# Kernel tuning notes

Hardware: AMD Instinct MI355X
Metric: run time of the kernel (lower is better)

Reference implementation:

```python
import jax, jax.numpy as jnp
import numpy as np

B, DIM, RANK, H, W = 16, 64, 32, 128, 128
E, K, BINS, FREQ_DIM, KS = 4, 2, 8, 64, 7
NOISE_STD = 1.0 / E


def dwconv(x, w, b, pad):
    # depthwise conv, NCHW, weight [C,1,kh,kw]
    y = jax.lax.conv_general_dilated(x, w, (1, 1), [(pad, pad), (pad, pad)],
        dimension_numbers=('NCHW', 'OIHW', 'NCHW'), feature_group_count=x.shape[1])
    return y + b[None, :, None, None]


def avgpool3(x):
    # AvgPool2d(3, stride=1, padding=1), count_include_pad=True -> sum/9
    s = jax.lax.reduce_window(x, 0.0, jax.lax.add, (1, 1, 3, 3), (1, 1, 1, 1),
        [(0, 0), (0, 0), (1, 1), (1, 1)])
    return s / 9.0


def freq_filter(x, gain, decay, cmax):
    # HighFreqGlobal / LowFreqGlobal: rfft2 -> scale magnitude by radial filter -> irfft2
    Bh, C, Hh, Wh = x.shape
    xf = jnp.fft.rfft2(x, norm='ortho')
    mag, ph = jnp.abs(xf), jnp.angle(xf)
    fy = jnp.fft.fftfreq(Hh).astype(x.dtype)[:, None]
    fx = jnp.fft.rfftfreq(Wh).astype(x.dtype)[None, :]
    fg = jnp.sqrt(fy ** 2 + fx ** 2)
    filt = jnp.clip((1.0 - jnp.exp(-gain * fg)) * jnp.exp(-decay * fg), 0.0, cmax)
    return jnp.fft.irfft2((mag * filt) * jnp.exp(1j * ph), s=(Hh, Wh), norm='ortho')


def freq_energy(x):
    # RoutingFunction.get_frequency_energy: radial energy histogram over BINS bins
    Bh, C, Hh, Wh = x.shape
    mag = jnp.abs(jnp.fft.fft2(x, norm='forward'))
    gy = jnp.arange(-Hh // 2, Hh // 2, dtype=jnp.float32)[:, None]
    gx = jnp.arange(-Wh // 2, Wh // 2, dtype=jnp.float32)[None, :]
    dist = jnp.sqrt(gy ** 2 + gx ** 2)
    edges = jnp.linspace(0.0, dist.max(), BINS + 1)
    masks = ((dist[None] >= edges[:-1, None, None]) & (dist[None] < edges[1:, None, None])).astype(mag.dtype)
    return jnp.einsum('bchw,khw->bk', mag, masks) / C  # sum over HW then mean over C


def setup_inputs():
    key = jax.random.key(0)
    ks = jax.random.split(key, 16)
    p = lambda k, shp, s=0.02: jax.random.normal(k, shp, jnp.float32) * s
    return {
        'x': jax.random.normal(ks[0], (B, DIM, H, W), jnp.float32),
        'noise': jax.random.normal(ks[1], (B, E), jnp.float32),
        'gate_w': p(ks[2], (E, DIM)),
        'fg_w1': p(ks[3], (FREQ_DIM, BINS)),
        'fg_b1': jnp.zeros((FREQ_DIM,), jnp.float32),
        'fg_w2': p(ks[4], (E, FREQ_DIM)),
        'proj0': p(ks[5], (E, RANK, DIM)),
        'proj1': p(ks[6], (E, RANK, DIM)),
        'proj2': p(ks[7], (E, DIM, RANK)),
        'hg_gain': jnp.float32(2.0),
        'hg_decay': jnp.float32(0.5),
        'hf_w1': p(ks[8], (RANK, 1, 3, 3), 0.1),
        'hf_b1': jnp.zeros((RANK,), jnp.float32),
        'hf_w2': p(ks[9], (RANK, 1, 3, 3), 0.1),
        'hf_b2': jnp.zeros((RANK,), jnp.float32),
        'lg_gain': jnp.float32(1.0),
        'lg_decay': jnp.float32(1.0),
        'lf_w': p(ks[10], (RANK, 1, KS, KS), 0.1),
        'lf_b': jnp.zeros((RANK,), jnp.float32),
    }


def reference(x, noise, gate_w, fg_w1, fg_b1, fg_w2, proj0, proj1, proj2,
              hg_gain, hg_decay, hf_w1, hf_b1, hf_w2, hf_b2,
              lg_gain, lg_decay, lf_w, lf_b):
    Bh = x.shape[0]
    # routing: image gate (GAP + linear) + frequency gate (MLP on radial energy)
    img_logits = jnp.mean(x, axis=(2, 3)) @ gate_w.T
    femb = freq_energy(x)
    hidden = jax.nn.relu(femb @ fg_w1.T + fg_b1)
    logits = img_logits + hidden @ fg_w2.T
    scores = jax.nn.softmax(logits + noise * NOISE_STD, axis=-1)
    vals, idx = jax.lax.top_k(scores, K)
    gates = jnp.zeros_like(scores).at[jnp.arange(Bh)[:, None], idx].set(vals)

    def expert(e, body):
        # ModExpert.process: low-rank proj -> body * silu(gate proj of shared=x) -> up proj + shortcut
        h = jnp.einsum('bchw,rc->brhw', x, proj0[e])
        g = jax.nn.silu(jnp.einsum('bchw,rc->brhw', x, proj1[e]))
        h = body(h) * g
        return jnp.einsum('brhw,cr->bchw', h, proj2[e]) + x

    gelu = lambda z: jax.nn.gelu(z, approximate=False)
    bodies = [
        lambda z: freq_filter(z, hg_gain, hg_decay, 3.0),                          # HighFreqGlobal
        lambda z: dwconv(gelu(dwconv(z, hf_w1, hf_b1, 1)), hf_w2, hf_b2, 1),       # HighFreqLocal
        lambda z: freq_filter(z, lg_gain, lg_decay, 1.0),                          # LowFreqGlobal
        lambda z: avgpool3(gelu(dwconv(z, lf_w, lf_b, KS // 2))),                  # LowFreqLocal
    ]
    # dispatch/combine expressed densely: gates are exactly zero for non-selected experts,
    # so weighted sum == SparseDispatcher.combine
    out = jnp.zeros_like(x)
    for e, body in enumerate(bodies):
        out = out + gates[:, e][:, None, None, None] * expert(e, body)
    return out
```

## Files before the change

kernel.cpp:

```cpp
#include <hip/hip_runtime.h>
#include <math.h>


namespace {

struct cpx { float x, y; };
struct TwB {
  cpx t0;
  cpx ws[6];
  float sg[6];
};

using bf16x8 = __attribute__((ext_vector_type(8))) short;
using f32x4  = __attribute__((ext_vector_type(4))) float;

__device__ __forceinline__ short f2bf(float f){
  unsigned u = __float_as_uint(f);
  u += 0x7FFF + ((u >> 16) & 1);
  return (short)(u >> 16);
}

__device__ __forceinline__ cpx cmul(cpx a, cpx b){ return {a.x*b.x - a.y*b.y, a.x*b.y + a.y*b.x}; }

__device__ __forceinline__ void init_twb(TwB &T, int lane, const float2* __restrict__ tw128){
  float2 v0 = tw128[lane];
  T.t0 = {v0.x, v0.y};
  int m = 32;
  #pragma unroll
  for (int s = 0; s < 6; s++){
    bool up = (lane & m) != 0;
    float2 wv = tw128[(lane & (m-1)) * (64/m)];
    T.ws[s] = up ? cpx{wv.x, wv.y} : cpx{1.0f, 0.0f};
    T.sg[s] = up ? -1.0f : 1.0f;
    m >>= 1;
  }
}

__device__ __forceinline__ int br6(int l){ return (int)(__brev((unsigned)l) >> 26); }
__device__ __forceinline__ int pos7(int j){ return ((j & 1) << 6) | (j >> 1); }

__device__ __forceinline__ void fft128(cpx &a, cpx &b, int lane, const TwB &T){
  cpx u{a.x + b.x, a.y + b.y};
  cpx v{a.x - b.x, a.y - b.y};
  v = cmul(v, T.t0);
  a = u; b = v;
  int m = 32;
  #pragma unroll
  for (int s = 0; s < 6; s++){
    float pax = __shfl_xor(a.x, m);
    float pay = __shfl_xor(a.y, m);
    float pbx = __shfl_xor(b.x, m);
    float pby = __shfl_xor(b.y, m);
    float sg = T.sg[s];
    cpx w = T.ws[s];
    cpx ta{fmaf(sg, a.x, pax), fmaf(sg, a.y, pay)};
    cpx tb{fmaf(sg, b.x, pbx), fmaf(sg, b.y, pby)};
    a = cmul(ta, w);
    b = cmul(tb, w);
    m >>= 1;
  }
}

__device__ __forceinline__ float gelu_exact(float v){
  return 0.5f * v * (1.0f + erff(v * 0.70710678118654752f));
}

__device__ __forceinline__ float silu(float v){
  return v / (1.0f + expf(-v));
}


__global__ __launch_bounds__(512) void k_fft2fwd(const float* __restrict__ x, float2* __restrict__ X,
                                                 float* __restrict__ part_w, float* __restrict__ xmean){
  __shared__ float2 z[8192];
  int bc = blockIdx.x; int t = threadIdx.x;
  int lane = t & 63, wv = t >> 6;
  if (t < 128){
    float s, c;
    sincosf(-6.283185307179586f * (float)t * (1.0f/128.0f), &s, &c);
    z[t] = make_float2(c, s);
  }
  __syncthreads();
  TwB T; init_twb(T, lane, (const float2*)z);
  __syncthreads();
  const float* img = x + (size_t)bc * 16384;
  int rb = br6(lane);

  #pragma unroll 4
  for (int k = 0; k < 8; k++){
    int p = wv*8 + k;
    int h0 = 2*p, h1 = 2*p + 1;
    cpx a{img[h0*128 + lane],      img[h1*128 + lane]};
    cpx b{img[h0*128 + lane + 64], img[h1*128 + lane + 64]};
    fft128(a, b, lane, T);
    int ia = (p << 7) | (rb ^ p);
    z[ia]      = make_float2(a.x, a.y);
    z[ia | 64] = make_float2(b.x, b.y);
  }
  __syncthreads();

  float rax[8], ray[8], rbx[8], rby[8];
  #pragma unroll
  for (int k = 0; k < 8; k++){
    int jj = wv*8 + k;
    int p  = lane >> 1, s = lane & 1;
    int p2 = 32 + p;
    cpx a, b;
    if (jj == 0){
      float2 z0  = z[(p << 7)  | (0  ^ p)];
      float2 z64 = z[(p << 7)  | (32 ^ p)];
      float2 w0  = z[(p2 << 7) | (0  ^ p2)];
      float2 w64 = z[(p2 << 7) | (32 ^ p2)];
      a = { s ? z0.y : z0.x, s ? z64.y : z64.x };
      b = { s ? w0.y : w0.x, s ? w64.y : w64.x };
    } else {
      int jm = 128 - jj;
      int pj = pos7(jj), pm = pos7(jm);
      float2 z1 = z[(p << 7) | (pj ^ p)],  z2 = z[(p << 7) | (pm ^ p)];
      if (s == 0) a = { 0.5f*(z1.x + z2.x), 0.5f*(z1.y - z2.y) };
      else        a = { 0.5f*(z1.y + z2.y), 0.5f*(z2.x - z1.x) };
      float2 w1 = z[(p2 << 7) | (pj ^ p2)], w2 = z[(p2 << 7) | (pm ^ p2)];
      if (s == 0) b = { 0.5f*(w1.x + w2.x), 0.5f*(w1.y - w2.y) };
      else        b = { 0.5f*(w1.y + w2.y), 0.5f*(w2.x - w1.x) };
    }
    fft128(a, b, lane, T);
    rax[k] = a.x; ray[k] = a.y; rbx[k] = b.x; rby[k] = b.y;
  }
  __syncthreads();
  #pragma unroll
  for (int k = 0; k < 8; k++){
    int jj = wv*8 + k;
    int ia = (jj << 7) | (rb ^ jj);
    z[ia]      = make_float2(rax[k], ray[k]);
    z[ia | 64] = make_float2(rbx[k], rby[k]);
  }
  __syncthreads();

  if (t == 0) xmean[bc] = z[0].x * (1.0f/16384.0f);

  float edges[9];
  float step = sqrtf(8192.0f) * 0.125f;
  #pragma unroll
  for (int k = 0; k <= 8; k++) edges[k] = step * (float)k;
  float acc[8] = {0,0,0,0,0,0,0,0};
  for (int idx = t; idx < 64*128; idx += 512){
    int j = idx >> 7, i = idx & 127;
    if (j == 0){
      float2 c0 = z[pos7(i)];
      int in_ = (128 - i) & 127;
      float2 d0v = z[pos7(in_)];
      float x0r = 0.5f*(c0.x + d0v.x), x0i = 0.5f*(c0.y - d0v.y);
      float x6r = 0.5f*(c0.y + d0v.y), x6i = 0.5f*(d0v.x - c0.x);
      float m0 = sqrtf(x0r*x0r + x0i*x0i) * (1.0f/16384.0f);
      float m6 = sqrtf(x6r*x6r + x6i*x6i) * (1.0f/16384.0f);
      float dyv = (float)(i - 64);
      float d0 = sqrtf(dyv*dyv + 4096.0f);
      float d6 = fabsf(dyv);
      #pragma unroll
      for (int k = 0; k < 8; k++){
        if (d0 >= edges[k] && d0 < edges[k+1]) acc[k] += m0;
        if (d6 >= edges[k] && d6 < edges[k+1]) acc[k] += m6;
      }
    } else {
      float2 zv = z[(j << 7) | (pos7(i) ^ j)];
      float mag = sqrtf(zv.x*zv.x + zv.y*zv.y) * (2.0f/16384.0f);
      float dy = (float)(i - 64), dx = (float)(j - 64);
      float d = sqrtf(dy*dy + dx*dx);
      #pragma unroll
      for (int k = 0; k < 8; k++)
        if (d >= edges[k] && d < edges[k+1]) acc[k] += mag;
    }
  }
  #pragma unroll
  for (int k = 0; k < 8; k++){
    float v = acc[k];
    for (int off = 32; off > 0; off >>= 1) v += __shfl_xor(v, off);
    if (lane == 0) part_w[(bc*8 + wv)*8 + k] = v;
  }

  float2* Xo = X + (size_t)bc * (65*128);
  for (int idx = t; idx < 65*128; idx += 512){
    int j = idx >> 7, i = idx & 127;
    float2 v;
    if (j == 0){
      float2 c0 = z[pos7(i)];
      int in_ = (128 - i) & 127;
      float2 d0v = z[pos7(in_)];
      v = make_float2(0.5f*(c0.x + d0v.x), 0.5f*(c0.y - d0v.y));
    } else if (j == 64){
      float2 c0 = z[pos7(i)];
      int in_ = (128 - i) & 127;
      float2 d0v = z[pos7(in_)];
      v = make_float2(0.5f*(c0.y + d0v.y), 0.5f*(d0v.x - c0.x));
    } else {
      v = z[(j << 7) | (pos7(i) ^ j)];
    }
    Xo[idx] = v;
  }
}

__global__ __launch_bounds__(128) void k_routing(const float* __restrict__ xmean, const float* __restrict__ part_w,
    const float* __restrict__ noise, const float* __restrict__ gate_w,
    const float* __restrict__ fg_w1, const float* __restrict__ fg_b1, const float* __restrict__ fg_w2,
    const float* __restrict__ proj0, float* __restrict__ p0t,
    int* __restrict__ slot_e, int* __restrict__ slot_of, float* __restrict__ slot_g){
  __shared__ float femb[16][8];
  __shared__ float hid[16][64];
  __shared__ float lgt[16][4];
  int t = threadIdx.x;
  for (int idx = t; idx < 2048; idx += 128){
    int r = idx >> 6, c = idx & 63;
    p0t[0*2048 + c*32 + r] = proj0[0*2048 + idx];
    p0t[1*2048 + c*32 + r] = proj0[2*2048 + idx];
  }
  {
    int b = t >> 3, k = t & 7;
    float s = 0.f;
    for (int c = 0; c < 64; c++)
      for (int w = 0; w < 8; w++)
        s += part_w[((b*64 + c)*8 + w)*8 + k];
    femb[b][k] = s * (1.0f/64.0f);
  }
  __syncthreads();
  for (int idx = t; idx < 16*64; idx += 128){
    int b = idx >> 6, f = idx & 63;
    float s = fg_b1[f];
    for (int k = 0; k < 8; k++) s += femb[b][k] * fg_w1[f*8 + k];
    hid[b][f] = fmaxf(s, 0.f);
  }
  __syncthreads();
  if (t < 64){
    int b = t >> 2, e = t & 3;
    float s = 0.f;
    for (int c = 0; c < 64; c++) s += xmean[b*64 + c] * gate_w[e*64 + c];
    for (int f = 0; f < 64; f++) s += hid[b][f] * fg_w2[e*64 + f];
    lgt[b][e] = s + noise[b*4 + e] * 0.25f;
  }
  __syncthreads();
  if (t < 16){
    int b = t;
    float m = fmaxf(fmaxf(lgt[b][0], lgt[b][1]), fmaxf(lgt[b][2], lgt[b][3]));
    float p[4]; float sum = 0.f;
    for (int e = 0; e < 4; e++){ p[e] = expf(lgt[b][e] - m); sum += p[e]; }
    for (int e = 0; e < 4; e++) p[e] /= sum;
    int i1 = 0;
    for (int e = 1; e < 4; e++) if (p[e] > p[i1]) i1 = e;
    int i2 = -1;
    for (int e = 0; e < 4; e++){ if (e == i1) continue; if (i2 < 0 || p[e] > p[i2]) i2 = e; }
    slot_e[b*2 + 0] = i1;
    slot_e[b*2 + 1] = i2;
    slot_g[b*2 + 0] = p[i1];
    slot_g[b*2 + 1] = p[i2];
    for (int e = 0; e < 4; e++) slot_of[b*4 + e] = (e == i1) ? 0 : ((e == i2) ? 1 : -1);
  }
}

__global__ __launch_bounds__(256) void k_projfreq(const float2* __restrict__ X, const float* __restrict__ p0t,
    float2* __restrict__ Y, const int* __restrict__ slot_e,
    const float* __restrict__ hg_gain, const float* __restrict__ hg_decay,
    const float* __restrict__ lg_gain, const float* __restrict__ lg_decay){
  int b = blockIdx.z;
  int e0 = __builtin_amdgcn_readfirstlane(slot_e[b*2 + 0]);
  int e1 = __builtin_amdgcn_readfirstlane(slot_e[b*2 + 1]);
  bool f0 = (e0 == 0) || (e0 == 2);
  bool f1 = (e1 == 0) || (e1 == 2);
  if (!f0 && !f1) return;
  int j = blockIdx.y;
  int i0 = blockIdx.x * 64;
  int t = threadIdx.x;
  int lane = t & 63;
  int w = __builtin_amdgcn_readfirstlane(t >> 6);
  __shared__ float2 sx[64][64];
  for (int idx = t; idx < 4096; idx += 256){
    int c = idx >> 6, ii = idx & 63;
    sx[c][ii] = X[(((size_t)(b*64 + c))*65 + j)*128 + i0 + ii];
  }
  __syncthreads();
  int i = i0 + lane;
  const float* W0 = p0t + ((f0 ? (e0 >> 1) : (e1 >> 1)) * 2048) + w*8;
  const float* W1 = p0t + ((f1 ? (e1 >> 1) : (e0 >> 1)) * 2048) + w*8;
  float a0x[8] = {0,0,0,0,0,0,0,0}, a0y[8] = {0,0,0,0,0,0,0,0};
  float a1x[8] = {0,0,0,0,0,0,0,0}, a1y[8] = {0,0,0,0,0,0,0,0};
  for (int c = 0; c < 64; c++){
    float2 xv = sx[c][lane];
    const float* wc0 = W0 + c*32;
    const float* wc1 = W1 + c*32;
    #pragma unroll
    for (int k = 0; k < 8; k++){
      float w0v = wc0[k];
      a0x[k] += w0v * xv.x; a0y[k] += w0v * xv.y;
      float w1v = wc1[k];
      a1x[k] += w1v * xv.x; a1y[k] += w1v * xv.y;
    }
  }
  float fy = (float)(i < 64 ? i : i - 128) * (1.0f/128.0f);
  float fx = (float)j * (1.0f/128.0f);
  float fg = sqrtf(fy*fy + fx*fx);
  if (f0){
    float gain, decay, cmax;
    if (e0 == 0){ gain = *hg_gain; decay = *hg_decay; cmax = 3.0f; }
    else        { gain = *lg_gain; decay = *lg_decay; cmax = 1.0f; }
    float filt = (1.0f - expf(-gain*fg)) * expf(-decay*fg);
    filt = fminf(fmaxf(filt, 0.0f), cmax) * (1.0f/16384.0f);
    int bs = b*2 + 0;
    #pragma unroll
    for (int k = 0; k < 8; k++){
      int r = w*8 + k;
      Y[((size_t)(bs*32 + r))*8320 + j*128 + i] = make_float2(a0x[k]*filt, a0y[k]*filt);
    }
  }
  if (f1){
    float gain, decay, cmax;
    if (e1 == 0){ gain = *hg_gain; decay = *hg_decay; cmax = 3.0f; }
    else        { gain = *lg_gain; decay = *lg_decay; cmax = 1.0f; }
    float filt = (1.0f - expf(-gain*fg)) * expf(-decay*fg);
    filt = fminf(fmaxf(filt, 0.0f), cmax) * (1.0f/16384.0f);
    int bs = b*2 + 1;
    #pragma unroll
    for (int k = 0; k < 8; k++){
      int r = w*8 + k;
      Y[((size_t)(bs*32 + r))*8320 + j*128 + i] = make_float2(a1x[k]*filt, a1y[k]*filt);
    }
  }
}

__global__ __launch_bounds__(512) void k_ifta(float2* __restrict__ Y, const int* __restrict__ slot_e,
    const float* __restrict__ x, const float* __restrict__ proj0, float* __restrict__ A){
  __shared__ __align__(16) unsigned char ubuf[65536];
  int bid = blockIdx.x;
  int t = threadIdx.x;
  if (bid < 1024){
    int bs = bid >> 5, r = bid & 31;
    int es = slot_e[bs];
    if (es == 1 || es == 3) return;
    float2* z = (float2*)ubuf;
    int lane = t & 63, wv = t >> 6;
    if (t < 128){
      float s, c;
      sincosf(-6.283185307179586f * (float)t * (1.0f/128.0f), &s, &c);
      z[t] = make_float2(c, s);
    }
    __syncthreads();
    TwB T; init_twb(T, lane, (const float2*)z);
    __syncthreads();
    int rb = br6(lane);
    float2* Yb = Y + (size_t)(bs*32 + r) * 8320;

    for (int idx = t; idx < 8192; idx += 512){
      int j = idx >> 7, i = idx & 127;
      if (j == 0){
        float2 y0 = Yb[i];
        float2 y6 = Yb[8192 + i];
        z[pos7(i)] = make_float2(y0.x - y6.y, y0.y + y6.x);
      } else {
        z[(j << 7) | (pos7(i) ^ j)] = Yb[idx];
      }
    }
    __syncthreads();

    #pragma unroll
    for (int k = 0; k < 8; k++){
      int jj = wv*8 + k;
      float2 z0 = z[(jj << 7) | (pos7(lane) ^ jj)];
      float2 z1 = z[(jj << 7) | ((pos7(lane) + 32) ^ jj)];
      cpx a{z0.x, -z0.y}, b{z1.x, -z1.y};
      fft128(a, b, lane, T);
      int ia = (jj << 7) | (rb ^ jj);
      z[ia]      = make_float2(a.x, -a.y);
      z[ia | 64] = make_float2(b.x, -b.y);
    }
    __syncthreads();

    float* body = (float*)Yb;
    #pragma unroll 2
    for (int k = 0; k < 8; k++){
      int p = wv*8 + k;
      int h = 2*p, h1 = 2*p + 1;
      int ph = pos7(h), ph1 = pos7(h1);
      cpx a, b;
      if (lane == 0){
        float2 c0 = z[ph], c1 = z[ph1];
        a = { c0.x, c1.x };
        b = { c0.y, c1.y };
      } else {
        float2 yh = z[(lane << 7) | (ph ^ lane)];
        float2 y1 = z[(lane << 7) | (ph1 ^ lane)];
        a = { yh.x - y1.y, yh.y + y1.x };
        int lm = 64 - lane;
        float2 zh  = z[(lm << 7) | (ph ^ lm)];
        float2 z1_ = z[(lm << 7) | (ph1 ^ lm)];
        b = { zh.x + z1_.y, z1_.x - zh.y };
      }
      a.y = -a.y; b.y = -b.y;
      fft128(a, b, lane, T);
      int n0 = 2*rb;
      body[h*128 + n0]      = a.x;
      body[h1*128 + n0]     = -a.y;
      body[h*128 + n0 + 1]  = b.x;
      body[h1*128 + n0 + 1] = -b.y;
    }
  } else {
    int aid = bid - 1024;
    int b = aid >> 6;
    int e0 = __builtin_amdgcn_readfirstlane(slot_e[b*2 + 0]);
    int e1 = __builtin_amdgcn_readfirstlane(slot_e[b*2 + 1]);
    bool c0 = (e0 == 1) || (e0 == 3);
    bool c1 = (e1 == 1) || (e1 == 3);
    if (!c0 && !c1) return;
    unsigned short (*xs)[72] = (unsigned short(*)[72])ubuf;
    int px0 = (aid & 63) * 256;
    int w = t >> 6, lane = t & 63;
    int h = lane & 15, g = lane >> 4;
    const float* xb = x + (size_t)b*64*16384;

    for (int idx = t; idx < 4096; idx += 512){
      int c = idx >> 6, pq = idx & 63;
      float4 v = *(const float4*)&xb[(size_t)c*16384 + px0 + pq*4];
      xs[pq*4 + 0][c] = (unsigned short)f2bf(v.x);
      xs[pq*4 + 1][c] = (unsigned short)f2bf(v.y);
      xs[pq*4 + 2][c] = (unsigned short)f2bf(v.z);
      xs[pq*4 + 3][c] = (unsigned short)f2bf(v.w);
    }

    bf16x8 af[2][2][2];
    #pragma unroll
    for (int s = 0; s < 2; s++){
      bool cv = (s == 0) ? c0 : c1;
      if (!cv) continue;
      int e = (s == 0) ? e0 : e1;
      const float* P0 = proj0 + e*2048;
      #pragma unroll
      for (int mr = 0; mr < 2; mr++)
        #pragma unroll
        for (int k0 = 0; k0 < 2; k0++){
          const float* p = P0 + (mr*16 + h)*64 + k0*32 + g*8;
          bf16x8 v;
          #pragma unroll
          for (int j = 0; j < 8; j++) v[j] = f2bf(p[j]);
          af[s][mr][k0] = v;
        }
    }
    __syncthreads();

    int pxw = w*32;
    #pragma unroll
    for (int nt = 0; nt < 2; nt++){
      int pxl = pxw + nt*16;
      int px  = px0 + pxl;
      bf16x8 bx[2];
      #pragma unroll
      for (int k0 = 0; k0 < 2; k0++)
        bx[k0] = *(bf16x8*)&xs[pxl + h][k0*32 + g*8];
      #pragma unroll
      for (int s = 0; s < 2; s++){
        bool cv = (s == 0) ? c0 : c1;
        if (!cv) continue;
        float* Ab = A + (size_t)((b*2 + s)*32)*16384;
        #pragma unroll
        for (int mr = 0; mr < 2; mr++){
          f32x4 acc = {0.f, 0.f, 0.f, 0.f};
          acc = __builtin_amdgcn_mfma_f32_16x16x32_bf16(af[s][mr][0], bx[0], acc, 0, 0, 0);
          acc = __builtin_amdgcn_mfma_f32_16x16x32_bf16(af[s][mr][1], bx[1], acc, 0, 0, 0);
          #pragma unroll
          for (int reg = 0; reg < 4; reg++){
            int r = mr*16 + g*4 + reg;
            Ab[(size_t)r*16384 + px + h] = acc[reg];
          }
        }
      }
    }
  }
}

__global__ __launch_bounds__(256) void k_conv(const float* __restrict__ A, float* __restrict__ bodyY,
    const float* __restrict__ w1g, const float* __restrict__ b1g,
    const float* __restrict__ w2g, const float* __restrict__ b2g,
    const float* __restrict__ wg, const float* __restrict__ bg,
    const int* __restrict__ slot_of){
  __shared__ __align__(16) float cbuf[5680];
  int by = blockIdx.y; int b = by >> 5, r = by & 31;
  int h0 = blockIdx.x * 16;
  int t = threadIdx.x;
  if (blockIdx.z == 0){
    int slot = slot_of[b*4 + 1];
    if (slot < 0) return;
    int bs = b*2 + slot;
    float* sin_ = cbuf;
    float* st   = cbuf + 2600;
    for (int i = t; i < 20*130; i += 256) sin_[i] = 0.f;
    for (int i = t; i < 18*130; i += 256) st[i] = 0.f;
    float w1[9], w2[9];
    #pragma unroll
    for (int k = 0; k < 9; k++){ w1[k] = w1g[r*9 + k]; w2[k] = w2g[r*9 + k]; }
    float b1 = b1g[r], b2 = b2g[r];
    __syncthreads();
    const float* ip = A + (size_t)(bs*32 + r)*16384;
    for (int idx = t; idx < 20*128; idx += 256){
      int li = idx >> 7, ww = idx & 127;
      int ih = h0 - 2 + li;
      if (ih >= 0 && ih < 128) sin_[li*130 + 1 + ww] = ip[ih*128 + ww];
    }
    __syncthreads();
    for (int idx = t; idx < 18*128; idx += 256){
      int li = idx >> 7, ww = idx & 127;
      int hs = h0 - 1 + li;
      if (hs >= 0 && hs < 128){
        float acc = b1;
        #pragma unroll
        for (int kh = 0; kh < 3; kh++)
          #pragma unroll
          for (int kw = 0; kw < 3; kw++)
            acc += w1[kh*3 + kw] * sin_[(li + kh)*130 + ww + kw];
        st[li*130 + 1 + ww] = gelu_exact(acc);
      }
    }
    __syncthreads();
    float* op = bodyY + (size_t)(bs*32 + r)*16640;
    for (int idx = t; idx < 16*128; idx += 256){
      int li = idx >> 7, ww = idx & 127;
      int ho = h0 + li;
      float acc = b2;
      #pragma unroll
      for (int kh = 0; kh < 3; kh++)
        #pragma unroll
        for (int kw = 0; kw < 3; kw++)
          acc += w2[kh*3 + kw] * st[(li + kh)*130 + ww + kw];
      op[ho*128 + ww] = acc;
    }
  } else {
    int slot = slot_of[b*4 + 3];
    if (slot < 0) return;
    int bs = b*2 + slot;
    float* sin_ = cbuf;
    float* st   = cbuf + 3216;
    float* wsh  = cbuf + 5628;
    for (int i = t; i < 24*134; i += 256) sin_[i] = 0.f;
    for (int i = t; i < 18*134; i += 256) st[i] = 0.f;
    if (t < 49) wsh[t] = wg[r*49 + t];
    float bias = bg[r];
    __syncthreads();
    const float* ip = A + (size_t)(bs*32 + r)*16384;
    for (int idx = t; idx < 24*128; idx += 256){
      int li = idx >> 7, ww = idx & 127;
      int ih = h0 - 4 + li;
      if (ih >= 0 && ih < 128) sin_[li*134 + 3 + ww] = ip[ih*128 + ww];
    }
    __syncthreads();
    for (int idx = t; idx < 18*128; idx += 256){
      int li = idx >> 7, ww = idx & 127;
      int hs = h0 - 1 + li;
      if (hs >= 0 && hs < 128){
        float acc = bias;
        #pragma unroll
        for (int kh = 0; kh < 7; kh++)
          #pragma unroll
          for (int kw = 0; kw < 7; kw++)
            acc += wsh[kh*7 + kw] * sin_[(li + kh)*134 + ww + kw];
        st[li*134 + 1 + ww] = gelu_exact(acc);
      }
    }
    __syncthreads();
    float* op = bodyY + (size_t)(bs*32 + r)*16640;
    for (int idx = t; idx < 16*128; idx += 256){
      int li = idx >> 7, ww = idx & 127;
      int ho = h0 + li;
      float acc = 0.f;
      #pragma unroll
      for (int kh = 0; kh < 3; kh++)
        #pragma unroll
        for (int kw = 0; kw < 3; kw++)
          acc += st[(li + kh)*134 + ww + kw];
      op[ho*128 + ww] = acc * (1.0f/9.0f);
    }
  }
}

__global__ __launch_bounds__(256) void k_combine(const float* __restrict__ x, const float* __restrict__ bodyY,
    const float* __restrict__ proj1, const float* __restrict__ proj2,
    const int* __restrict__ slot_e, const float* __restrict__ slot_g,
    float* __restrict__ out){
  __shared__ __align__(16) unsigned char smem[57344];
  unsigned short (*xs)[72]            = (unsigned short(*)[72])(smem);
  unsigned short (*bs2)[128][36]      = (unsigned short(*)[128][36])(smem + 18432);
  unsigned short (*sblk)[4][2][16][40] = (unsigned short(*)[4][2][16][40])(smem + 36864);
  float* obuf = (float*)smem;

  int b = blockIdx.y;
  int px0 = blockIdx.x * 128;
  int t = threadIdx.x;
  int w = t >> 6, lane = t & 63;
  int h = lane & 15, g = lane >> 4;
  int ea = __builtin_amdgcn_readfirstlane(slot_e[b*2 + 0]);
  int eb = __builtin_amdgcn_readfirstlane(slot_e[b*2 + 1]);
  float ga = slot_g[b*2 + 0], gb = slot_g[b*2 + 1];
  float gs = ga + gb;

  const float* xb = x + (size_t)b*64*16384;
  float* ob = out + (size_t)b*64*16384;
  const float* Bd0 = bodyY + (size_t)(b*2 + 0)*32*16640;
  const float* Bd1 = bodyY + (size_t)(b*2 + 1)*32*16640;

  for (int idx = t; idx < 2048; idx += 256){
    int c = idx >> 5, pq = idx & 31;
    float4 v = *(const float4*)&xb[(size_t)c*16384 + px0 + pq*4];
    xs[pq*4 + 0][c] = (unsigned short)f2bf(v.x);
    xs[pq*4 + 1][c] = (unsigned short)f2bf(v.y);
    xs[pq*4 + 2][c] = (unsigned short)f2bf(v.z);
    xs[pq*4 + 3][c] = (unsigned short)f2bf(v.w);
  }
  for (int idx = t; idx < 2048; idx += 256){
    int s = idx >> 10, r = (idx >> 5) & 31, pq = idx & 31;
    const float* Bod = (s == 0) ? Bd0 : Bd1;
    float4 v = *(const float4*)&Bod[(size_t)r*16640 + px0 + pq*4];
    bs2[s][pq*4 + 0][r] = (unsigned short)f2bf(v.x);
    bs2[s][pq*4 + 1][r] = (unsigned short)f2bf(v.y);
    bs2[s][pq*4 + 2][r] = (unsigned short)f2bf(v.z);
    bs2[s][pq*4 + 3][r] = (unsigned short)f2bf(v.w);
  }

  bf16x8 a1[2][2][2];
  #pragma unroll
  for (int s = 0; s < 2; s++){
    const float* P1 = proj1 + (s == 0 ? ea : eb)*2048;
    #pragma unroll
    for (int mr = 0; mr < 2; mr++)
      #pragma unroll
      for (int k0 = 0; k0 < 2; k0++){
        const float* p = P1 + (mr*16 + h)*64 + k0*32 + g*8;
        bf16x8 v;
        #pragma unroll
        for (int j = 0; j < 8; j++) v[j] = f2bf(p[j]);
        a1[s][mr][k0] = v;
      }
  }
  bf16x8 a2[2][4];
  #pragma unroll
  for (int s = 0; s < 2; s++){
    const float* P2 = proj2 + (s == 0 ? ea : eb)*2048;
    #pragma unroll
    for (int mc = 0; mc < 4; mc++){
      const float* p = P2 + (mc*16 + h)*32 + g*8;
      bf16x8 v;
      #pragma unroll
      for (int j = 0; j < 8; j++) v[j] = f2bf(p[j]);
      a2[s][mc] = v;
    }
  }
  __syncthreads();

  int pxw = w*32;
  #pragma unroll
  for (int nt = 0; nt < 2; nt++){
    int pxl = pxw + nt*16;
    bf16x8 bx[2];
    #pragma unroll
    for (int k0 = 0; k0 < 2; k0++)
      bx[k0] = *(bf16x8*)&xs[pxl + h][k0*32 + g*8];
    f32x4 acc1[2][2];
    #pragma unroll
    for (int s = 0; s < 2; s++)
      #pragma unroll
      for (int mr = 0; mr < 2; mr++){
        f32x4 acc = {0.f, 0.f, 0.f, 0.f};
        acc = __builtin_amdgcn_mfma_f32_16x16x32_bf16(a1[s][mr][0], bx[0], acc, 0, 0, 0);
        acc = __builtin_amdgcn_mfma_f32_16x16x32_bf16(a1[s][mr][1], bx[1], acc, 0, 0, 0);
        acc1[s][mr] = acc;
      }
    #pragma unroll
    for (int s = 0; s < 2; s++){
      float gw = (s == 0) ? ga : gb;
      #pragma unroll
      for (int mr = 0; mr < 2; mr++){
        int r0 = mr*16 + g*4;
        unsigned short b4[4];
        *(uint2*)b4 = *(uint2*)&bs2[s][pxl + h][r0];
        unsigned pk0, pk1;
        {
          float bv0 = __uint_as_float(((unsigned)b4[0]) << 16);
          float bv1 = __uint_as_float(((unsigned)b4[1]) << 16);
          float bv2 = __uint_as_float(((unsigned)b4[2]) << 16);
          float bv3 = __uint_as_float(((unsigned)b4[3]) << 16);
          float s0 = gw * bv0 * silu(acc1[s][mr][0]);
          float s1 = gw * bv1 * silu(acc1[s][mr][1]);
          float s2 = gw * bv2 * silu(acc1[s][mr][2]);
          float s3 = gw * bv3 * silu(acc1[s][mr][3]);
          pk0 = (unsigned)(unsigned short)f2bf(s0) | ((unsigned)(unsigned short)f2bf(s1) << 16);
          pk1 = (unsigned)(unsigned short)f2bf(s2) | ((unsigned)(unsigned short)f2bf(s3) << 16);
        }
        uint2 pv; pv.x = pk0; pv.y = pk1;
        *(uint2*)&sblk[nt][w][s][h][r0] = pv;
      }
    }
  }
  __syncthreads();

  #pragma unroll
  for (int nt = 0; nt < 2; nt++){
    bf16x8 sb0 = *(bf16x8*)&sblk[nt][w][0][h][g*8];
    bf16x8 sb1 = *(bf16x8*)&sblk[nt][w][1][h][g*8];
    #pragma unroll
    for (int mc = 0; mc < 4; mc++){
      f32x4 acc = {0.f, 0.f, 0.f, 0.f};
      acc = __builtin_amdgcn_mfma_f32_16x16x32_bf16(a2[0][mc], sb0, acc, 0, 0, 0);
      acc = __builtin_amdgcn_mfma_f32_16x16x32_bf16(a2[1][mc], sb1, acc, 0, 0, 0);
      #pragma unroll
      for (int reg = 0; reg < 4; reg++){
        int c = mc*16 + g*4 + reg;
        obuf[(w*64 + c)*36 + nt*16 + h] = acc[reg];
      }
    }
  }
  int fq = lane & 7, cr = lane >> 3;
  const float* xw = xb + px0 + w*32;
  float* ow = ob + px0 + w*32;
  #pragma unroll
  for (int i = 0; i < 8; i++){
    int c = i*8 + cr;
    float4 v = *(float4*)&obuf[(w*64 + c)*36 + fq*4];
    float4 xv4 = *(const float4*)&xw[(size_t)c*16384 + fq*4];
    *(float4*)&ow[(size_t)c*16384 + fq*4] =
      make_float4(gs*xv4.x + v.x, gs*xv4.y + v.y, gs*xv4.z + v.z, gs*xv4.w + v.w);
  }
}

}

extern "C" void kernel_launch(void* const* d_in, const int* in_sizes, int n_in,
                              void* d_out, int out_size, void* d_ws, size_t ws_size,
                              hipStream_t stream) {
  (void)in_sizes; (void)n_in; (void)out_size; (void)ws_size;
  const float* x        = (const float*)d_in[0];
  const float* noise    = (const float*)d_in[1];
  const float* gate_w   = (const float*)d_in[2];
  const float* fg_w1    = (const float*)d_in[3];
  const float* fg_b1    = (const float*)d_in[4];
  const float* fg_w2    = (const float*)d_in[5];
  const float* proj0    = (const float*)d_in[6];
  const float* proj1    = (const float*)d_in[7];
  const float* proj2    = (const float*)d_in[8];
  const float* hg_gain  = (const float*)d_in[9];
  const float* hg_decay = (const float*)d_in[10];
  const float* hf_w1    = (const float*)d_in[11];
  const float* hf_b1    = (const float*)d_in[12];
  const float* hf_w2    = (const float*)d_in[13];
  const float* hf_b2    = (const float*)d_in[14];
  const float* lg_gain  = (const float*)d_in[15];
  const float* lg_decay = (const float*)d_in[16];
  const float* lf_w     = (const float*)d_in[17];
  const float* lf_b     = (const float*)d_in[18];
  float* out = (float*)d_out;

  float* ws = (float*)d_ws;
  float2* X  = (float2*)ws;
  float*  A  = ws;
  float*  Yf = ws + 17039360;
  float2* Y2 = (float2*)Yf;
  float*  tail   = ws + 34078720;
  float*  xmean  = tail;
  float*  part_w = xmean + 1024;
  float*  p0t    = part_w + 65536;
  float*  slot_g = p0t + 4096;
  int*    slot_e = (int*)(slot_g + 32);
  int*    slot_of = slot_e + 32;

  k_fft2fwd<<<1024, 512, 0, stream>>>(x, X, part_w, xmean);
  k_routing<<<1, 128, 0, stream>>>(xmean, part_w, noise, gate_w, fg_w1, fg_b1, fg_w2,
                                   proj0, p0t, slot_e, slot_of, slot_g);
  k_projfreq<<<dim3(2,65,16), 256, 0, stream>>>(X, p0t, Y2, slot_e,
                                                hg_gain, hg_decay, lg_gain, lg_decay);
  k_ifta<<<2048, 512, 0, stream>>>(Y2, slot_e, x, proj0, A);
  k_conv<<<dim3(8,512,2), 256, 0, stream>>>(A, Yf, hf_w1, hf_b1, hf_w2, hf_b2,
                                            lf_w, lf_b, slot_of);
  k_combine<<<dim3(128,16), 256, 0, stream>>>(x, Yf, proj1, proj2, slot_e, slot_g, out);
}
```

Measured before the change: 299.3 us.

## Halve combine tile to 64 pixels and write output directly from MFMA results

The combine kernel now handles 64 pixels per block instead of 128, giving one 16-pixel tile per wave and twice as many blocks. The LDS footprint shrinks because the float output staging buffer is gone. Results are written straight to global memory from the MFMA accumulators, and the second __syncthreads is dropped since each wave only reads back its own sblk slice. The trade-off is that the global stores and x reads are now 16-pixel-wide scattered accesses per channel instead of coalesced float4, and the proj1/proj2 weight loads are repeated across twice as many blocks.

```diff
diff --git a/kernel.cpp b/kernel.cpp
--- a/kernel.cpp
+++ b/kernel.cpp
@@ -579,14 +579,11 @@
     const float* __restrict__ proj1, const float* __restrict__ proj2,
     const int* __restrict__ slot_e, const float* __restrict__ slot_g,
     float* __restrict__ out){
-  __shared__ __align__(16) unsigned char smem[57344];
-  unsigned short (*xs)[72]            = (unsigned short(*)[72])(smem);
-  unsigned short (*bs2)[128][36]      = (unsigned short(*)[128][36])(smem + 18432);
-  unsigned short (*sblk)[4][2][16][40] = (unsigned short(*)[4][2][16][40])(smem + 36864);
-  float* obuf = (float*)smem;
-
+  __shared__ unsigned short xs[64][72];
+  __shared__ unsigned short bs2[2][64][36];
+  __shared__ unsigned short sblk[4][2][16][40];
   int b = blockIdx.y;
-  int px0 = blockIdx.x * 128;
+  int px0 = blockIdx.x * 64;
   int t = threadIdx.x;
   int w = t >> 6, lane = t & 63;
   int h = lane & 15, g = lane >> 4;
@@ -600,16 +597,16 @@
   const float* Bd0 = bodyY + (size_t)(b*2 + 0)*32*16640;
   const float* Bd1 = bodyY + (size_t)(b*2 + 1)*32*16640;
 
-  for (int idx = t; idx < 2048; idx += 256){
-    int c = idx >> 5, pq = idx & 31;
+  for (int idx = t; idx < 1024; idx += 256){
+    int c = idx >> 4, pq = idx & 15;
     float4 v = *(const float4*)&xb[(size_t)c*16384 + px0 + pq*4];
     xs[pq*4 + 0][c] = (unsigned short)f2bf(v.x);
     xs[pq*4 + 1][c] = (unsigned short)f2bf(v.y);
     xs[pq*4 + 2][c] = (unsigned short)f2bf(v.z);
     xs[pq*4 + 3][c] = (unsigned short)f2bf(v.w);
   }
-  for (int idx = t; idx < 2048; idx += 256){
-    int s = idx >> 10, r = (idx >> 5) & 31, pq = idx & 31;
+  for (int idx = t; idx < 1024; idx += 256){
+    int s = idx >> 9, r = (idx >> 4) & 31, pq = idx & 15;
     const float* Bod = (s == 0) ? Bd0 : Bd1;
     float4 v = *(const float4*)&Bod[(size_t)r*16640 + px0 + pq*4];
     bs2[s][pq*4 + 0][r] = (unsigned short)f2bf(v.x);
@@ -648,79 +645,65 @@
   }
   __syncthreads();
 
-  int pxw = w*32;
-  #pragma unroll
-  for (int nt = 0; nt < 2; nt++){
-    int pxl = pxw + nt*16;
-    bf16x8 bx[2];
-    #pragma unroll
-    for (int k0 = 0; k0 < 2; k0++)
-      bx[k0] = *(bf16x8*)&xs[pxl + h][k0*32 + g*8];
-    f32x4 acc1[2][2];
-    #pragma unroll
-    for (int s = 0; s < 2; s++)
-      #pragma unroll
-      for (int mr = 0; mr < 2; mr++){
-        f32x4 acc = {0.f, 0.f, 0.f, 0.f};
-        acc = __builtin_amdgcn_mfma_f32_16x16x32_bf16(a1[s][mr][0], bx[0], acc, 0, 0, 0);
-        acc = __builtin_amdgcn_mfma_f32_16x16x32_bf16(a1[s][mr][1], bx[1], acc, 0, 0, 0);
-        acc1[s][mr] = acc;
+  int pxl = w*16;
+  int px  = px0 + pxl;
+  bf16x8 bx[2];
+  #pragma unroll
+  for (int k0 = 0; k0 < 2; k0++)
+    bx[k0] = *(bf16x8*)&xs[pxl + h][k0*32 + g*8];
+  f32x4 acc1[2][2];
+  #pragma unroll
+  for (int s = 0; s < 2; s++)
+    #pragma unroll
+    for (int mr = 0; mr < 2; mr++){
+      f32x4 acc = {0.f, 0.f, 0.f, 0.f};
+      acc = __builtin_amdgcn_mfma_f32_16x16x32_bf16(a1[s][mr][0], bx[0], acc, 0, 0, 0);
+      acc = __builtin_amdgcn_mfma_f32_16x16x32_bf16(a1[s][mr][1], bx[1], acc, 0, 0, 0);
+      acc1[s][mr] = acc;
+    }
+  #pragma unroll
+  for (int s = 0; s < 2; s++){
+    float gw = (s == 0) ? ga : gb;
+    #pragma unroll
+    for (int mr = 0; mr < 2; mr++){
+      int r0 = mr*16 + g*4;
+      unsigned short b4[4];
+      *(uint2*)b4 = *(uint2*)&bs2[s][pxl + h][r0];
+      unsigned pk0, pk1;
+      {
+        float bv0 = __uint_as_float(((unsigned)b4[0]) << 16);
+        float bv1 = __uint_as_float(((unsigned)b4[1]) << 16);
+        float bv2 = __uint_as_float(((unsigned)b4[2]) << 16);
+        float bv3 = __uint_as_float(((unsigned)b4[3]) << 16);
+        float s0 = gw * bv0 * silu(acc1[s][mr][0]);
+        float s1 = gw * bv1 * silu(acc1[s][mr][1]);
+        float s2 = gw * bv2 * silu(acc1[s][mr][2]);
+        float s3 = gw * bv3 * silu(acc1[s][mr][3]);
+        pk0 = (unsigned)(unsigned short)f2bf(s0) | ((unsigned)(unsigned short)f2bf(s1) << 16);
+        pk1 = (unsigned)(unsigned short)f2bf(s2) | ((unsigned)(unsigned short)f2bf(s3) << 16);
       }
-    #pragma unroll
-    for (int s = 0; s < 2; s++){
-      float gw = (s == 0) ? ga : gb;
-      #pragma unroll
-      for (int mr = 0; mr < 2; mr++){
-        int r0 = mr*16 + g*4;
-        unsigned short b4[4];
-        *(uint2*)b4 = *(uint2*)&bs2[s][pxl + h][r0];
-        unsigned pk0, pk1;
-        {
-          float bv0 = __uint_as_float(((unsigned)b4[0]) << 16);
-          float bv1 = __uint_as_float(((unsigned)b4[1]) << 16);
-          float bv2 = __uint_as_float(((unsigned)b4[2]) << 16);
-          float bv3 = __uint_as_float(((unsigned)b4[3]) << 16);
-          float s0 = gw * bv0 * silu(acc1[s][mr][0]);
-          float s1 = gw * bv1 * silu(acc1[s][mr][1]);
-          float s2 = gw * bv2 * silu(acc1[s][mr][2]);
-          float s3 = gw * bv3 * silu(acc1[s][mr][3]);
-          pk0 = (unsigned)(unsigned short)f2bf(s0) | ((unsigned)(unsigned short)f2bf(s1) << 16);
-          pk1 = (unsigned)(unsigned short)f2bf(s2) | ((unsigned)(unsigned short)f2bf(s3) << 16);
-        }
-        uint2 pv; pv.x = pk0; pv.y = pk1;
-        *(uint2*)&sblk[nt][w][s][h][r0] = pv;
-      }
-    }
-  }
-  __syncthreads();
-
-  #pragma unroll
-  for (int nt = 0; nt < 2; nt++){
-    bf16x8 sb0 = *(bf16x8*)&sblk[nt][w][0][h][g*8];
-    bf16x8 sb1 = *(bf16x8*)&sblk[nt][w][1][h][g*8];
-    #pragma unroll
-    for (int mc = 0; mc < 4; mc++){
-      f32x4 acc = {0.f, 0.f, 0.f, 0.f};
-      acc = __builtin_amdgcn_mfma_f32_16x16x32_bf16(a2[0][mc], sb0, acc, 0, 0, 0);
-      acc = __builtin_amdgcn_mfma_f32_16x16x32_bf16(a2[1][mc], sb1, acc, 0, 0, 0);
-      #pragma unroll
-      for (int reg = 0; reg < 4; reg++){
-        int c = mc*16 + g*4 + reg;
-        obuf[(w*64 + c)*36 + nt*16 + h] = acc[reg];
-      }
-    }
-  }
-  int fq = lane & 7, cr = lane >> 3;
-  const float* xw = xb + px0 + w*32;
-  float* ow = ob + px0 + w*32;
-  #pragma unroll
-  for (int i = 0; i < 8; i++){
-    int c = i*8 + cr;
-    float4 v = *(float4*)&obuf[(w*64 + c)*36 + fq*4];
-    float4 xv4 = *(const float4*)&xw[(size_t)c*16384 + fq*4];
-    *(float4*)&ow[(size_t)c*16384 + fq*4] =
-      make_float4(gs*xv4.x + v.x, gs*xv4.y + v.y, gs*xv4.z + v.z, gs*xv4.w + v.w);
-  }
+      uint2 pv; pv.x = pk0; pv.y = pk1;
+      *(uint2*)&sblk[w][s][h][r0] = pv;
+    }
+  }
+  bf16x8 sb0 = *(bf16x8*)&sblk[w][0][h][g*8];
+  bf16x8 sb1 = *(bf16x8*)&sblk[w][1][h][g*8];
+  f32x4 acc2[4];
+  #pragma unroll
+  for (int mc = 0; mc < 4; mc++){
+    f32x4 acc = {0.f, 0.f, 0.f, 0.f};
+    acc = __builtin_amdgcn_mfma_f32_16x16x32_bf16(a2[0][mc], sb0, acc, 0, 0, 0);
+    acc = __builtin_amdgcn_mfma_f32_16x16x32_bf16(a2[1][mc], sb1, acc, 0, 0, 0);
+    acc2[mc] = acc;
+  }
+  #pragma unroll
+  for (int mc = 0; mc < 4; mc++)
+    #pragma unroll
+    for (int reg = 0; reg < 4; reg++){
+      int c = mc*16 + g*4 + reg;
+      size_t o = (size_t)c*16384 + px + h;
+      ob[o] = gs * xb[o] + acc2[mc][reg];
+    }
 }
 
 }
@@ -771,5 +754,5 @@
   k_ifta<<<2048, 512, 0, stream>>>(Y2, slot_e, x, proj0, A);
   k_conv<<<dim3(8,512,2), 256, 0, stream>>>(A, Yf, hf_w1, hf_b1, hf_w2, hf_b2,
                                             lf_w, lf_b, slot_of);
-  k_combine<<<dim3(128,16), 256, 0, stream>>>(x, Yf, proj1, proj2, slot_e, slot_g, out);
-}
+  k_combine<<<dim3(256,16), 256, 0, stream>>>(x, Yf, proj1, proj2, slot_e, slot_g, out);
+}
```

Result: slower. 307.4 us (+2.7%).
